# Kernel optimization log

Hardware: AMD Instinct MI355X
Metric: run time of the kernel (lower is better)

The kernel has to match this reference:

```python
import jax, jax.numpy as jnp
import numpy as np

N = 50000      # nodes
E = 800000     # edges
IN = 128       # in_channels
HID = 32       # hidden_channels per head
HEADS = 4
OUT = 16       # out_channels
NEG_SLOPE_ATT = 0.2   # GATv2Conv default negative_slope
NEG_SLOPE_ACT = 0.01  # F.leaky_relu default
EPS = 1e-16


def setup_inputs() -> dict:
    key = jax.random.key(0)
    ks = jax.random.split(key, 13)
    d1 = HEADS * HID  # 128
    g = lambda k, shape, fan: jax.random.normal(k, shape, jnp.float32) * (1.0 / np.sqrt(fan))
    return {
        "x": jax.random.normal(ks[0], (N, IN), jnp.float32),
        "edge_index": jax.random.randint(ks[1], (2, E), 0, N, dtype=jnp.int32),
        "edge_weight": jax.random.uniform(ks[2], (E,), jnp.float32),
        # conv1 (GATv2): lin_l, lin_r, att, bias
        "Wl1": g(ks[3], (IN, d1), IN), "Wr1": g(ks[4], (IN, d1), IN),
        "att1": g(ks[5], (HEADS, HID), HID), "b1": jnp.zeros((d1,), jnp.float32),
        # conv2
        "Wl2": g(ks[6], (d1, d1), d1), "Wr2": g(ks[7], (d1, d1), d1),
        "att2": g(ks[8], (HEADS, HID), HID), "b2": jnp.zeros((d1,), jnp.float32),
        # classifier
        "Wc": g(ks[9], (d1, OUT), d1), "bc": jnp.zeros((OUT,), jnp.float32),
    }


def gatv2_layer(x, Wl, Wr, att, bias, src, dst):
    n = x.shape[0]
    xl = (x @ Wl).reshape(n, HEADS, HID)  # source transform
    xr = (x @ Wr).reshape(n, HEADS, HID)  # target transform
    m = xl[src] + xr[dst]                                    # [Etot, H, C]
    e = jnp.sum(jax.nn.leaky_relu(m, NEG_SLOPE_ATT) * att, axis=-1)  # [Etot, H]
    # segment softmax over incoming edges of each target node
    emax = jax.ops.segment_max(e, dst, num_segments=n)       # [N, H]
    ex = jnp.exp(e - emax[dst])
    denom = jax.ops.segment_sum(ex, dst, num_segments=n)     # [N, H]
    alpha = ex / (denom[dst] + EPS)                          # [Etot, H]
    out = jax.ops.segment_sum(xl[src] * alpha[:, :, None], dst, num_segments=n)  # [N, H, C]
    return out.reshape(n, HEADS * HID) + bias


def reference(x, edge_index, edge_weight, Wl1, Wr1, att1, b1, Wl2, Wr2, att2, b2, Wc, bc):
    # GATv2Conv default add_self_loops=True
    loops = jnp.arange(N, dtype=edge_index.dtype)
    src = jnp.concatenate([edge_index[0], loops])
    dst = jnp.concatenate([edge_index[1], loops])
    h = gatv2_layer(x, Wl1, Wr1, att1, b1, src, dst)
    h = jax.nn.leaky_relu(h, NEG_SLOPE_ACT)
    h = gatv2_layer(h, Wl2, Wr2, att2, b2, src, dst)
    h = jax.nn.leaky_relu(h, NEG_SLOPE_ACT)
    logits = h @ Wc + bc
    return (logits, h)
```

## Files before the change

kernel.cpp:

```cpp
#include <hip/hip_runtime.h>
#include <hip/hip_fp16.h>


#define LOG2E 1.4426950408889634f
#define AST 40

typedef short bf16x8 __attribute__((ext_vector_type(8)));
typedef float f32x4 __attribute__((ext_vector_type(4)));

__device__ __forceinline__ unsigned short f2bf(float f) {
  union { float f; unsigned u; } x; x.f = f;
  unsigned r = x.u + 0x7fffu + ((x.u >> 16) & 1u);
  return (unsigned short)(r >> 16);
}
__device__ __forceinline__ float bf2f(unsigned short h) {
  union { unsigned u; float f; } x; x.u = ((unsigned)h) << 16;
  return x.f;
}
__device__ __forceinline__ void split4(float4 v, ushort4& h, ushort4& l) {
  h.x = f2bf(v.x); l.x = f2bf(v.x - bf2f(h.x));
  h.y = f2bf(v.y); l.y = f2bf(v.y - bf2f(h.y));
  h.z = f2bf(v.z); l.z = f2bf(v.z - bf2f(h.z));
  h.w = f2bf(v.w); l.w = f2bf(v.w - bf2f(h.w));
}


__global__ __launch_bounds__(256) void scan_blk(const int* __restrict__ cnt,
                                                int* __restrict__ excl,
                                                int* __restrict__ bsum, int n) {
  __shared__ int s[256];
  int t = threadIdx.x, i = blockIdx.x * 256 + t;
  int v = (i < n) ? (cnt[i] + 1) : 0;
  s[t] = v;
  __syncthreads();
#pragma unroll
  for (int off = 1; off < 256; off <<= 1) {
    int u = (t >= off) ? s[t - off] : 0;
    __syncthreads();
    s[t] += u;
    __syncthreads();
  }
  if (i < n) excl[i] = s[t] - v;
  if (t == 255) bsum[blockIdx.x] = s[255];
}

__global__ __launch_bounds__(256) void scan_bsum(int* __restrict__ bsum, int nb,
                                                 int* __restrict__ row_start, int n) {
  __shared__ int s[256];
  int t = threadIdx.x;
  int v = (t < nb) ? bsum[t] : 0;
  s[t] = v;
  __syncthreads();
#pragma unroll
  for (int off = 1; off < 256; off <<= 1) {
    int u = (t >= off) ? s[t - off] : 0;
    __syncthreads();
    s[t] += u;
    __syncthreads();
  }
  if (t < nb) bsum[t] = s[t] - v;
  if (t == 255) row_start[n] = s[255];
}

__global__ __launch_bounds__(256) void scan_add(int* __restrict__ row_start,
                                                const int* __restrict__ bsum,
                                                int* __restrict__ wpos,
                                                int* __restrict__ csr,
                                                int n, int padBase) {
  int i = blockIdx.x * 256 + threadIdx.x;
  if (i < n) {
    int r = row_start[i] + bsum[blockIdx.x];
    row_start[i] = r;
    wpos[i] = r + 1;
    csr[r] = i;
  }
  if (blockIdx.x == 0 && threadIdx.x < 16) csr[padBase + threadIdx.x] = 0;
}

#define EPB 1024
__global__ __launch_bounds__(256) void convert_count(
    const float* __restrict__ Wl1, const float* __restrict__ Wr1,
    const float* __restrict__ Wl2, const float* __restrict__ Wr2,
    unsigned short* __restrict__ BT1h, unsigned short* __restrict__ BT1l,
    unsigned short* __restrict__ BT2h, unsigned short* __restrict__ BT2l,
    const int* __restrict__ esrc, const int* __restrict__ edst,
    int* __restrict__ cnt, int* __restrict__ bucketCur,
    int2* __restrict__ bucket, int E, int sliceSize, int cap) {
  int b = blockIdx.x;
  int t = threadIdx.x;
  if (b >= 256) {
    __shared__ int bcnt[8], bbase[8];
    if (t < 8) bcnt[t] = 0;
    __syncthreads();
    int base = (b - 256) * EPB;
    int sl[4], rk[4], dv[4], sv[4];
#pragma unroll
    for (int j = 0; j < 4; ++j) {
      int i = base + t + j * 256;
      bool v = (i < E);
      int d = v ? edst[i] : 0;
      sv[j] = v ? esrc[i] : 0;
      dv[j] = d;
      int s = d / sliceSize;
      sl[j] = v ? s : -1;
      if (v) {
        atomicAdd(&cnt[d], 1);
        rk[j] = atomicAdd(&bcnt[s], 1);
      }
    }
    __syncthreads();
    if (t < 8 && bcnt[t] > 0) bbase[t] = atomicAdd(&bucketCur[t], bcnt[t]);
    __syncthreads();
#pragma unroll
    for (int j = 0; j < 4; ++j) {
      if (sl[j] >= 0) {
        int pos = sl[j] * cap + bbase[sl[j]] + rk[j];
        bucket[pos] = make_int2(sv[j], dv[j]);
      }
    }
    return;
  }
  const float* Wl = (b < 128) ? Wl1 : Wl2;
  const float* Wr = (b < 128) ? Wr1 : Wr2;
  unsigned short* BTh = (b < 128) ? BT1h : BT2h;
  unsigned short* BTl = (b < 128) ? BT1l : BT2l;
  int idx = (b & 127) * 256 + t;
  int col = idx >> 7, k = idx & 127;
  float v = (col < 128) ? Wl[k * 128 + col] : Wr[k * 128 + (col - 128)];
  unsigned short h = f2bf(v);
  BTh[idx] = h;
  BTl[idx] = f2bf(v - bf2f(h));
}

enum { IN_F32 = 0, IN_F16 = 1 };
#define NSCAT 1152
#define NCHUNK 128
template <int MODE, int FUSE>
__global__ __launch_bounds__(256) void gemm_mfma(
    const float* __restrict__ Af, const __half* __restrict__ Af16,
    const unsigned short* __restrict__ BTh, const unsigned short* __restrict__ BTl,
    __half* __restrict__ Cl, __half* __restrict__ Cr, int nrows,
    const int2* __restrict__ bucket, const int* __restrict__ bucketCur,
    int* __restrict__ wpos, int* __restrict__ csr, int cap) {
  __shared__ __align__(16) unsigned short smem[4 * 128 * AST];
  int tid = threadIdx.x;
  int bx, by;
  if (FUSE) {
    int g = blockIdx.x / 9, r = blockIdx.x - g * 9;
    if (r < 5) {
      int sid = g * 5 + r;
      if (sid < NSCAT) {
        int slice = blockIdx.x & 7;
        int chunk = (g >> 3) * 5;
        for (int gp = g & ~7; gp < g; ++gp)
          chunk += (((slice - gp) & 7) < 5) ? 1 : 0;
        if (chunk < NCHUNK) {
          int cntS = bucketCur[slice];
          int per = (cntS + NCHUNK - 1) / NCHUNK;
          int b0 = chunk * per;
          int ee = min(b0 + per, cntS);
          const int2* bk = bucket + (size_t)slice * cap;
          int i = b0 + tid;
          for (; i + 256 < ee; i += 512) {
            int2 e0 = bk[i];
            int2 e1 = bk[i + 256];
            int p0 = atomicAdd(&wpos[e0.y], 1); csr[p0] = e0.x;
            int p1 = atomicAdd(&wpos[e1.y], 1); csr[p1] = e1.x;
          }
          for (; i < ee; i += 256) {
            int2 e = bk[i];
            int p = atomicAdd(&wpos[e.y], 1); csr[p] = e.x;
          }
        }
      }
      return;
    }
    int gid = g * 4 + (r - 5);
    int nbx = (nrows + 127) >> 7;
    if (gid >= nbx * 2) return;
    bx = gid >> 1;
    by = gid & 1;
  } else {
    bx = blockIdx.x;
    by = blockIdx.y;
  }

  unsigned short* sAh = smem;
  unsigned short* sAl = smem + 5120;
  unsigned short* sBh = smem + 10240;
  unsigned short* sBl = smem + 15360;

  int wave = tid >> 6, lane = tid & 63;
  int rowBase = bx * 128;
  int colBase = by * 128;
  int rowHalf = (wave >> 1) * 64;
  int colHalf = (wave & 1) * 64;
  int l15 = lane & 15, quad = lane >> 4;

  f32x4 acc[4][4];
#pragma unroll
  for (int m = 0; m < 4; ++m)
#pragma unroll
    for (int n = 0; n < 4; ++n) acc[m][n] = (f32x4){0.f, 0.f, 0.f, 0.f};

  for (int kc = 0; kc < 4; ++kc) {
#pragma unroll
    for (int i = 0; i < 2; ++i) {
      int idx = tid + i * 256;
      int row = idx >> 2, seg = idx & 3;
      int gr = rowBase + row;
      float4 v0 = make_float4(0.f, 0.f, 0.f, 0.f), v1 = v0;
      if (MODE == IN_F32) {
        if (gr < nrows) {
          v0 = *(const float4*)&Af[(size_t)gr * 128 + kc * 32 + seg * 8];
          v1 = *(const float4*)&Af[(size_t)gr * 128 + kc * 32 + seg * 8 + 4];
        }
      } else {
        if (gr < nrows) {
          uint4 raw = *(const uint4*)&Af16[(size_t)gr * 128 + kc * 32 + seg * 8];
          const __half* hp = (const __half*)&raw;
          v0 = make_float4(__half2float(hp[0]), __half2float(hp[1]),
                           __half2float(hp[2]), __half2float(hp[3]));
          v1 = make_float4(__half2float(hp[4]), __half2float(hp[5]),
                           __half2float(hp[6]), __half2float(hp[7]));
        }
      }
      ushort4 h0, l0, h1, l1;
      split4(v0, h0, l0);
      split4(v1, h1, l1);
      *(ushort4*)&sAh[row * AST + seg * 8] = h0;
      *(ushort4*)&sAh[row * AST + seg * 8 + 4] = h1;
      *(ushort4*)&sAl[row * AST + seg * 8] = l0;
      *(ushort4*)&sAl[row * AST + seg * 8 + 4] = l1;
    }
#pragma unroll
    for (int i = 0; i < 2; ++i) {
      int idx = tid + i * 256;
      int col = idx >> 2, seg = idx & 3;
      *(uint4*)&sBh[col * AST + seg * 8] =
          *(const uint4*)&BTh[(size_t)(colBase + col) * 128 + kc * 32 + seg * 8];
      *(uint4*)&sBl[col * AST + seg * 8] =
          *(const uint4*)&BTl[(size_t)(colBase + col) * 128 + kc * 32 + seg * 8];
    }
    __syncthreads();

    bf16x8 afh[4], afl[4], bfh[4], bfl[4];
#pragma unroll
    for (int m = 0; m < 4; ++m) {
      int r = rowHalf + m * 16 + l15;
      afh[m] = *(const bf16x8*)&sAh[r * AST + quad * 8];
      afl[m] = *(const bf16x8*)&sAl[r * AST + quad * 8];
    }
#pragma unroll
    for (int n = 0; n < 4; ++n) {
      int cc = colHalf + n * 16 + l15;
      bfh[n] = *(const bf16x8*)&sBh[cc * AST + quad * 8];
      bfl[n] = *(const bf16x8*)&sBl[cc * AST + quad * 8];
    }
    __builtin_amdgcn_s_setprio(1);
#pragma unroll
    for (int m = 0; m < 4; ++m)
#pragma unroll
      for (int n = 0; n < 4; ++n) {
        acc[m][n] = __builtin_amdgcn_mfma_f32_16x16x32_bf16(afh[m], bfh[n], acc[m][n], 0, 0, 0);
        acc[m][n] = __builtin_amdgcn_mfma_f32_16x16x32_bf16(afh[m], bfl[n], acc[m][n], 0, 0, 0);
        acc[m][n] = __builtin_amdgcn_mfma_f32_16x16x32_bf16(afl[m], bfh[n], acc[m][n], 0, 0, 0);
      }
    __builtin_amdgcn_s_setprio(0);
    __syncthreads();
  }

  __half* __restrict__ C = (by == 0) ? Cl : Cr;
#pragma unroll
  for (int m = 0; m < 4; ++m)
#pragma unroll
    for (int r = 0; r < 4; ++r) {
      int grow = rowBase + rowHalf + m * 16 + quad * 4 + r;
      if (grow < nrows) {
#pragma unroll
        for (int n = 0; n < 4; ++n)
          C[(size_t)grow * 128 + colHalf + n * 16 + l15] = __float2half(acc[m][n][r]);
      }
    }
}

__global__ __launch_bounds__(256) void gat_attn(const __half* __restrict__ xl,
                                                const __half* __restrict__ xr,
                                                const int* __restrict__ row_start,
                                                const int* __restrict__ csr,
                                                const float* __restrict__ att,
                                                const float* __restrict__ bias,
                                                float* __restrict__ ofp,
                                                __half* __restrict__ oh16,
                                                int n_nodes) {
  int node = blockIdx.x * 4 + (threadIdx.x >> 6);
  if (node >= n_nodes) return;
  int lane = threadIdx.x & 63;
  int slot = lane >> 4;
  int l15 = lane & 15;
  int c0 = l15 * 8;

  float fxr[8];
  {
    uint4 raw = *(const uint4*)&xr[(size_t)node * 128 + c0];
    const __half* hp = (const __half*)&raw;
#pragma unroll
    for (int k = 0; k < 8; ++k) fxr[k] = __half2float(hp[k]);
  }
  float a06[8], a04[8];
  {
    float4 a0 = *(const float4*)&att[c0];
    float4 a1 = *(const float4*)&att[c0 + 4];
    float av[8] = {a0.x, a0.y, a0.z, a0.w, a1.x, a1.y, a1.z, a1.w};
    const float C06 = 0.6f * LOG2E, C04 = 0.4f * LOG2E;
#pragma unroll
    for (int k = 0; k < 8; ++k) { a06[k] = av[k] * C06; a04[k] = av[k] * C04; }
  }

  float acc[8];
#pragma unroll
  for (int k = 0; k < 8; ++k) acc[k] = 0.f;
  float lsum = 0.f;

#define EDGE_BODY(SRC, PVALID)                                                 \
  {                                                                            \
    uint4 raw = *(const uint4*)&xl[(size_t)(unsigned)(SRC)*128 + c0];          \
    const __half* hp = (const __half*)&raw;                                    \
    float e = 0.f;                                                             \
    _Pragma("unroll") for (int k = 0; k < 8; ++k) {                            \
      float t = __half2float(hp[k]) + fxr[k];                                  \
      e = fmaf(a06[k], t, e);                                                  \
      e = fmaf(a04[k], fabsf(t), e);                                           \
    }                                                                          \
    e += __shfl_xor(e, 1);                                                     \
    e += __shfl_xor(e, 2);                                                     \
    float p = (PVALID) ? __builtin_amdgcn_exp2f(e) : 0.f;                      \
    lsum += p;                                                                 \
    _Pragma("unroll") for (int k = 0; k < 8; ++k)                              \
        acc[k] = fmaf(p, __half2float(hp[k]), acc[k]);                         \
  }

  int beg = row_start[node], end = row_start[node + 1];
  int deg = end - beg;
  int fullEnd = beg + (deg & ~15);

  for (int base = beg; base < fullEnd; base += 16) {
    int b0 = base + 4 * slot;
    int s0 = csr[b0], s1 = csr[b0 + 1], s2 = csr[b0 + 2], s3 = csr[b0 + 3];
    EDGE_BODY(s0, true);
    EDGE_BODY(s1, true);
    EDGE_BODY(s2, true);
    EDGE_BODY(s3, true);
  }
  for (int base = fullEnd; base < end; base += 4) {
    int idx = base + slot;
    int src = csr[idx];
    EDGE_BODY(src, idx < end);
  }
#undef EDGE_BODY

  lsum += __shfl_xor(lsum, 16);
  lsum += __shfl_xor(lsum, 32);
#pragma unroll
  for (int k = 0; k < 8; ++k) {
    acc[k] += __shfl_xor(acc[k], 16);
    acc[k] += __shfl_xor(acc[k], 32);
  }

  if (slot == 0) {
    float4 b0v = *(const float4*)&bias[c0];
    float4 b1v = *(const float4*)&bias[c0 + 4];
    float bv[8] = {b0v.x, b0v.y, b0v.z, b0v.w, b1v.x, b1v.y, b1v.z, b1v.w};
    float inv = 1.f / (lsum + 1e-16f);
    float o[8];
#pragma unroll
    for (int k = 0; k < 8; ++k) {
      float v = fmaf(acc[k], inv, bv[k]);
      o[k] = fmaf(0.495f, fabsf(v), 0.505f * v);
    }
    if (ofp) {
      *(float4*)&ofp[(size_t)node * 128 + c0] = make_float4(o[0], o[1], o[2], o[3]);
      *(float4*)&ofp[(size_t)node * 128 + c0 + 4] = make_float4(o[4], o[5], o[6], o[7]);
    }
    if (oh16) {
      ushort4 ha, hb;
      ha.x = __half_as_ushort(__float2half(o[0]));
      ha.y = __half_as_ushort(__float2half(o[1]));
      ha.z = __half_as_ushort(__float2half(o[2]));
      ha.w = __half_as_ushort(__float2half(o[3]));
      hb.x = __half_as_ushort(__float2half(o[4]));
      hb.y = __half_as_ushort(__float2half(o[5]));
      hb.z = __half_as_ushort(__float2half(o[6]));
      hb.w = __half_as_ushort(__float2half(o[7]));
      *(ushort4*)&oh16[(size_t)node * 128 + c0] = ha;
      *(ushort4*)&oh16[(size_t)node * 128 + c0 + 4] = hb;
    }
  }
}

__global__ __launch_bounds__(256) void classifier_kernel(const float4* __restrict__ h4,
                                                         const float* __restrict__ Wc,
                                                         const float* __restrict__ bc,
                                                         float* __restrict__ logits,
                                                         int n) {
  __shared__ float sW[2048];
  __shared__ float sb[16];
  int t = threadIdx.x;
#pragma unroll
  for (int i = 0; i < 8; ++i) sW[t + i * 256] = Wc[t + i * 256];
  if (t < 16) sb[t] = bc[t];
  __syncthreads();
  int node = blockIdx.x * 256 + t;
  if (node >= n) return;
  float acc[16];
#pragma unroll
  for (int o = 0; o < 16; ++o) acc[o] = sb[o];
  for (int c4 = 0; c4 < 32; ++c4) {
    float4 hv = h4[(unsigned)node * 32 + c4];
    const float* w = &sW[c4 * 64];
#pragma unroll
    for (int o = 0; o < 16; ++o) {
      acc[o] = fmaf(hv.x, w[o], acc[o]);
      acc[o] = fmaf(hv.y, w[16 + o], acc[o]);
      acc[o] = fmaf(hv.z, w[32 + o], acc[o]);
      acc[o] = fmaf(hv.w, w[48 + o], acc[o]);
    }
  }
#pragma unroll
  for (int q = 0; q < 4; ++q)
    *(float4*)&logits[(size_t)node * 16 + q * 4] =
        make_float4(acc[q * 4], acc[q * 4 + 1], acc[q * 4 + 2], acc[q * 4 + 3]);
}


extern "C" void kernel_launch(void* const* d_in, const int* in_sizes, int n_in,
                              void* d_out, int out_size, void* d_ws, size_t ws_size,
                              hipStream_t stream) {
  const float* x    = (const float*)d_in[0];
  const int*   ei   = (const int*)d_in[1];
  const float* Wl1  = (const float*)d_in[3];
  const float* Wr1  = (const float*)d_in[4];
  const float* att1 = (const float*)d_in[5];
  const float* b1   = (const float*)d_in[6];
  const float* Wl2  = (const float*)d_in[7];
  const float* Wr2  = (const float*)d_in[8];
  const float* att2 = (const float*)d_in[9];
  const float* b2   = (const float*)d_in[10];
  const float* Wc   = (const float*)d_in[11];
  const float* bc   = (const float*)d_in[12];

  const int N = in_sizes[0] / 128;
  const int E = in_sizes[1] / 2;

  float* outp   = (float*)d_out;
  float* logits = outp;
  float* hout   = outp + (size_t)N * 16;
  __half* h1f16 = (__half*)hout;

  const int cap = E / 8 + 16384;

  char* ws = (char*)d_ws;
  __half* xlbuf = (__half*)ws;                ws += (size_t)N * 128 * 2;
  __half* xrbuf = (__half*)ws;                ws += (size_t)N * 128 * 2;
  unsigned short* WT1h = (unsigned short*)ws; ws += 256 * 128 * 2;
  unsigned short* WT1l = (unsigned short*)ws; ws += 256 * 128 * 2;
  unsigned short* WT2h = (unsigned short*)ws; ws += 256 * 128 * 2;
  unsigned short* WT2l = (unsigned short*)ws; ws += 256 * 128 * 2;
  int* cnt       = (int*)ws;                  ws += (size_t)N * 4;
  int* bucketCur = (int*)ws;                  ws += 8 * 4;
  int* wpos      = (int*)ws;                  ws += (size_t)N * 4;
  int* bsum      = (int*)ws;                  ws += 256 * 4;
  int2* bucket   = (int2*)ws;                 ws += (size_t)8 * cap * 8;
  int* row_start = (int*)ws;                  ws += (size_t)(N + 1) * 4;
  int* csr       = (int*)ws;                  ws += (size_t)(E + N + 16) * 4;

  const int* esrc = ei;
  const int* edst = ei + E;

  int gN = (N + 255) / 256;
  int gAttn = (N + 3) / 4;
  int sliceSize = (N + 7) / 8;

  int nbx = (N + 127) / 128;
  int nGemm = nbx * 2;
  int groups = (NSCAT + 4) / 5;
  int g2 = (nGemm + 3) / 4;
  if (g2 > groups) groups = g2;
  int gFused = groups * 9;

  hipMemsetAsync(cnt, 0, (size_t)(N + 8) * 4, stream);
  convert_count<<<256 + (E + EPB - 1) / EPB, 256, 0, stream>>>(
      Wl1, Wr1, Wl2, Wr2, WT1h, WT1l, WT2h, WT2l,
      esrc, edst, cnt, bucketCur, bucket, E, sliceSize, cap);
  scan_blk<<<gN, 256, 0, stream>>>(cnt, row_start, bsum, N);
  scan_bsum<<<1, 256, 0, stream>>>(bsum, gN, row_start, N);
  scan_add<<<gN, 256, 0, stream>>>(row_start, bsum, wpos, csr, N, E + N);

  gemm_mfma<IN_F32, 1><<<gFused, 256, 0, stream>>>(
      x, nullptr, WT1h, WT1l, xlbuf, xrbuf, N,
      bucket, bucketCur, wpos, csr, cap);
  gat_attn<<<gAttn, 256, 0, stream>>>(xlbuf, xrbuf, row_start, csr, att1, b1,
                                      nullptr, h1f16, N);

  gemm_mfma<IN_F16, 0><<<dim3(nbx, 2), 256, 0, stream>>>(
      nullptr, h1f16, WT2h, WT2l, xlbuf, xrbuf, N,
      nullptr, nullptr, nullptr, nullptr, 0);
  gat_attn<<<gAttn, 256, 0, stream>>>(xlbuf, xrbuf, row_start, csr, att2, b2,
                                      hout, nullptr, N);

  classifier_kernel<<<(N + 255) / 256, 256, 0, stream>>>((const float4*)hout, Wc, bc,
                                                         logits, N);
}
```

Baseline: 307.0 us.

## Interleave CSR edge scatter into GEMM blocks and merge the scan kernels

Previously the first GEMM launch had dedicated scatter blocks in a 5:4 interleave. Now every GEMM block preloads its share of the bucketed edges into registers before its k-loop. It issues the wpos atomics after the first k-iteration and the csr stores after the second, so the atomic latency hides behind MFMA work. Separately, the single-block scan_bsum kernel is removed: each scan_add block redundantly scans the block sums in shared memory, saving one launch. The per-block edge capacity is fixed at 5×256, so a slice with more edges than the grid can hold would silently drop edges. The extra registers held across the k-loop may also affect occupancy.

```diff
diff --git a/kernel.cpp b/kernel.cpp
--- a/kernel.cpp
+++ b/kernel.cpp
@@ -44,8 +44,11 @@
   if (t == 255) bsum[blockIdx.x] = s[255];
 }
 
-__global__ __launch_bounds__(256) void scan_bsum(int* __restrict__ bsum, int nb,
-                                                 int* __restrict__ row_start, int n) {
+__global__ __launch_bounds__(256) void scan_add(int* __restrict__ row_start,
+                                                const int* __restrict__ bsum,
+                                                int* __restrict__ wpos,
+                                                int* __restrict__ csr,
+                                                int n, int padBase, int nb) {
   __shared__ int s[256];
   int t = threadIdx.x;
   int v = (t < nb) ? bsum[t] : 0;
@@ -58,23 +61,18 @@
     s[t] += u;
     __syncthreads();
   }
-  if (t < nb) bsum[t] = s[t] - v;
-  if (t == 255) row_start[n] = s[255];
-}
-
-__global__ __launch_bounds__(256) void scan_add(int* __restrict__ row_start,
-                                                const int* __restrict__ bsum,
-                                                int* __restrict__ wpos,
-                                                int* __restrict__ csr,
-                                                int n, int padBase) {
-  int i = blockIdx.x * 256 + threadIdx.x;
+  int pref = (blockIdx.x > 0) ? s[blockIdx.x - 1] : 0;
+  int i = blockIdx.x * 256 + t;
   if (i < n) {
-    int r = row_start[i] + bsum[blockIdx.x];
+    int r = row_start[i] + pref;
     row_start[i] = r;
     wpos[i] = r + 1;
     csr[r] = i;
   }
-  if (blockIdx.x == 0 && threadIdx.x < 16) csr[padBase + threadIdx.x] = 0;
+  if (blockIdx.x == 0) {
+    if (t == 0) row_start[n] = s[nb - 1];
+    if (t < 16) csr[padBase + t] = 0;
+  }
 }
 
 #define EPB 1024
@@ -133,8 +131,7 @@
 }
 
 enum { IN_F32 = 0, IN_F16 = 1 };
-#define NSCAT 1152
-#define NCHUNK 128
+#define SJ 5
 template <int MODE, int FUSE>
 __global__ __launch_bounds__(256) void gemm_mfma(
     const float* __restrict__ Af, const __half* __restrict__ Af16,
@@ -145,39 +142,33 @@
   __shared__ __align__(16) unsigned short smem[4 * 128 * AST];
   int tid = threadIdx.x;
   int bx, by;
+  int2 ebuf[SJ];
+  int epos[SJ];
   if (FUSE) {
-    int g = blockIdx.x / 9, r = blockIdx.x - g * 9;
-    if (r < 5) {
-      int sid = g * 5 + r;
-      if (sid < NSCAT) {
-        int slice = blockIdx.x & 7;
-        int chunk = (g >> 3) * 5;
-        for (int gp = g & ~7; gp < g; ++gp)
-          chunk += (((slice - gp) & 7) < 5) ? 1 : 0;
-        if (chunk < NCHUNK) {
-          int cntS = bucketCur[slice];
-          int per = (cntS + NCHUNK - 1) / NCHUNK;
-          int b0 = chunk * per;
-          int ee = min(b0 + per, cntS);
-          const int2* bk = bucket + (size_t)slice * cap;
-          int i = b0 + tid;
-          for (; i + 256 < ee; i += 512) {
-            int2 e0 = bk[i];
-            int2 e1 = bk[i + 256];
-            int p0 = atomicAdd(&wpos[e0.y], 1); csr[p0] = e0.x;
-            int p1 = atomicAdd(&wpos[e1.y], 1); csr[p1] = e1.x;
-          }
-          for (; i < ee; i += 256) {
-            int2 e = bk[i];
-            int p = atomicAdd(&wpos[e.y], 1); csr[p] = e.x;
-          }
+    int gid = blockIdx.x;
+    int slice = gid & 7;
+    int rank = gid >> 3;
+    int nbs = (int)(gridDim.x >> 3);
+    int cntS = bucketCur[slice];
+    int per = (cntS + nbs - 1) / nbs;
+    int b0 = rank * per;
+    int ee = min(b0 + per, cntS);
+    const int2* bk = bucket + (size_t)slice * cap;
+#pragma unroll
+    for (int j = 0; j < SJ; ++j) {
+      int idx = b0 + tid + j * 256;
+      ebuf[j] = (idx < ee) ? bk[idx] : make_int2(0, -1);
+    }
+    int nbx = (nrows + 127) >> 7;
+    if (gid >= nbx * 2) {
+#pragma unroll
+      for (int j = 0; j < SJ; ++j)
+        if (ebuf[j].y >= 0) {
+          int p = atomicAdd(&wpos[ebuf[j].y], 1);
+          csr[p] = ebuf[j].x;
         }
-      }
       return;
     }
-    int gid = g * 4 + (r - 5);
-    int nbx = (nrows + 127) >> 7;
-    if (gid >= nbx * 2) return;
     bx = gid >> 1;
     by = gid & 1;
   } else {
@@ -268,6 +259,18 @@
       }
     __builtin_amdgcn_s_setprio(0);
     __syncthreads();
+
+    if (FUSE) {
+      if (kc == 0) {
+#pragma unroll
+        for (int j = 0; j < SJ; ++j)
+          epos[j] = (ebuf[j].y >= 0) ? atomicAdd(&wpos[ebuf[j].y], 1) : -1;
+      } else if (kc == 1) {
+#pragma unroll
+        for (int j = 0; j < SJ; ++j)
+          if (epos[j] >= 0) csr[epos[j]] = ebuf[j].x;
+      }
+    }
   }
 
   __half* __restrict__ C = (by == 0) ? Cl : Cr;
@@ -483,18 +486,14 @@
 
   int nbx = (N + 127) / 128;
   int nGemm = nbx * 2;
-  int groups = (NSCAT + 4) / 5;
-  int g2 = (nGemm + 3) / 4;
-  if (g2 > groups) groups = g2;
-  int gFused = groups * 9;
+  int gFused = (nGemm + 7) & ~7;
 
   hipMemsetAsync(cnt, 0, (size_t)(N + 8) * 4, stream);
   convert_count<<<256 + (E + EPB - 1) / EPB, 256, 0, stream>>>(
       Wl1, Wr1, Wl2, Wr2, WT1h, WT1l, WT2h, WT2l,
       esrc, edst, cnt, bucketCur, bucket, E, sliceSize, cap);
   scan_blk<<<gN, 256, 0, stream>>>(cnt, row_start, bsum, N);
-  scan_bsum<<<1, 256, 0, stream>>>(bsum, gN, row_start, N);
-  scan_add<<<gN, 256, 0, stream>>>(row_start, bsum, wpos, csr, N, E + N);
+  scan_add<<<gN, 256, 0, stream>>>(row_start, bsum, wpos, csr, N, E + N, gN);
 
   gemm_mfma<IN_F32, 1><<<gFused, 256, 0, stream>>>(
       x, nullptr, WT1h, WT1l, xlbuf, xrbuf, N,
```

Result: slower. 318.9 us (+3.9%).

## Switch split GEMM to fp16 MFMA, skip A-low term for fp16 input, merge scans

Applied to the files above, without the earlier changes.

Replaces the bf16 hi/lo split with an fp16 hi/lo split and uses fp16 MFMA. For the second-layer GEMM, whose input is already fp16, the A operand is copied directly to shared memory without conversion, dropping the A-low buffer and one of three MFMAs per tile. Separately, the block-sum scan is folded into scan_add: every block redundantly scans the block sums itself, saving one kernel launch. The risk is fp16 range and precision: weights and x whose magnitude exceeds fp16 range, or small residuals that underflow, could lose accuracy.

```diff
diff --git a/kernel.cpp b/kernel.cpp
--- a/kernel.cpp
+++ b/kernel.cpp
@@ -5,7 +5,7 @@
 #define LOG2E 1.4426950408889634f
 #define AST 40
 
-typedef short bf16x8 __attribute__((ext_vector_type(8)));
+typedef _Float16 f16x8 __attribute__((ext_vector_type(8)));
 typedef float f32x4 __attribute__((ext_vector_type(4)));
 
 __device__ __forceinline__ unsigned short f2bf(float f) {
@@ -17,11 +17,13 @@
   union { unsigned u; float f; } x; x.u = ((unsigned)h) << 16;
   return x.f;
 }
-__device__ __forceinline__ void split4(float4 v, ushort4& h, ushort4& l) {
-  h.x = f2bf(v.x); l.x = f2bf(v.x - bf2f(h.x));
-  h.y = f2bf(v.y); l.y = f2bf(v.y - bf2f(h.y));
-  h.z = f2bf(v.z); l.z = f2bf(v.z - bf2f(h.z));
-  h.w = f2bf(v.w); l.w = f2bf(v.w - bf2f(h.w));
+__device__ __forceinline__ void split4h(float4 v, ushort4& h, ushort4& l) {
+  __half hx = __float2half(v.x), hy = __float2half(v.y);
+  __half hz = __float2half(v.z), hw = __float2half(v.w);
+  h.x = __half_as_ushort(hx); l.x = __half_as_ushort(__float2half(v.x - __half2float(hx)));
+  h.y = __half_as_ushort(hy); l.y = __half_as_ushort(__float2half(v.y - __half2float(hy)));
+  h.z = __half_as_ushort(hz); l.z = __half_as_ushort(__float2half(v.z - __half2float(hz)));
+  h.w = __half_as_ushort(hw); l.w = __half_as_ushort(__float2half(v.w - __half2float(hw)));
 }
 
 
@@ -44,8 +46,11 @@
   if (t == 255) bsum[blockIdx.x] = s[255];
 }
 
-__global__ __launch_bounds__(256) void scan_bsum(int* __restrict__ bsum, int nb,
-                                                 int* __restrict__ row_start, int n) {
+__global__ __launch_bounds__(256) void scan_add(int* __restrict__ row_start,
+                                                const int* __restrict__ bsum,
+                                                int* __restrict__ wpos,
+                                                int* __restrict__ csr,
+                                                int n, int padBase, int nb) {
   __shared__ int s[256];
   int t = threadIdx.x;
   int v = (t < nb) ? bsum[t] : 0;
@@ -58,23 +63,18 @@
     s[t] += u;
     __syncthreads();
   }
-  if (t < nb) bsum[t] = s[t] - v;
-  if (t == 255) row_start[n] = s[255];
-}
-
-__global__ __launch_bounds__(256) void scan_add(int* __restrict__ row_start,
-                                                const int* __restrict__ bsum,
-                                                int* __restrict__ wpos,
-                                                int* __restrict__ csr,
-                                                int n, int padBase) {
-  int i = blockIdx.x * 256 + threadIdx.x;
+  int pref = (blockIdx.x > 0) ? s[blockIdx.x - 1] : 0;
+  int i = blockIdx.x * 256 + t;
   if (i < n) {
-    int r = row_start[i] + bsum[blockIdx.x];
+    int r = row_start[i] + pref;
     row_start[i] = r;
     wpos[i] = r + 1;
     csr[r] = i;
   }
-  if (blockIdx.x == 0 && threadIdx.x < 16) csr[padBase + threadIdx.x] = 0;
+  if (blockIdx.x == 0) {
+    if (t == 0) row_start[n] = s[nb - 1];
+    if (t < 16) csr[padBase + t] = 0;
+  }
 }
 
 #define EPB 1024
@@ -127,9 +127,9 @@
   int idx = (b & 127) * 256 + t;
   int col = idx >> 7, k = idx & 127;
   float v = (col < 128) ? Wl[k * 128 + col] : Wr[k * 128 + (col - 128)];
-  unsigned short h = f2bf(v);
-  BTh[idx] = h;
-  BTl[idx] = f2bf(v - bf2f(h));
+  __half h = __float2half(v);
+  BTh[idx] = __half_as_ushort(h);
+  BTl[idx] = __half_as_ushort(__float2half(v - __half2float(h)));
 }
 
 enum { IN_F32 = 0, IN_F16 = 1 };
@@ -142,7 +142,8 @@
     __half* __restrict__ Cl, __half* __restrict__ Cr, int nrows,
     const int2* __restrict__ bucket, const int* __restrict__ bucketCur,
     int* __restrict__ wpos, int* __restrict__ csr, int cap) {
-  __shared__ __align__(16) unsigned short smem[4 * 128 * AST];
+  constexpr int NBUF = (MODE == IN_F16) ? 3 : 4;
+  __shared__ __align__(16) unsigned short smem[NBUF * 128 * AST];
   int tid = threadIdx.x;
   int bx, by;
   if (FUSE) {
@@ -185,10 +186,11 @@
     by = blockIdx.y;
   }
 
+  constexpr int ABUF = 128 * AST;
   unsigned short* sAh = smem;
-  unsigned short* sAl = smem + 5120;
-  unsigned short* sBh = smem + 10240;
-  unsigned short* sBl = smem + 15360;
+  unsigned short* sAl = (MODE == IN_F32) ? smem + ABUF : nullptr;
+  unsigned short* sBh = smem + ((MODE == IN_F32) ? 2 * ABUF : ABUF);
+  unsigned short* sBl = smem + ((MODE == IN_F32) ? 3 * ABUF : 2 * ABUF);
 
   int wave = tid >> 6, lane = tid & 63;
   int rowBase = bx * 128;
@@ -209,29 +211,25 @@
       int idx = tid + i * 256;
       int row = idx >> 2, seg = idx & 3;
       int gr = rowBase + row;
-      float4 v0 = make_float4(0.f, 0.f, 0.f, 0.f), v1 = v0;
       if (MODE == IN_F32) {
+        float4 v0 = make_float4(0.f, 0.f, 0.f, 0.f), v1 = v0;
         if (gr < nrows) {
           v0 = *(const float4*)&Af[(size_t)gr * 128 + kc * 32 + seg * 8];
           v1 = *(const float4*)&Af[(size_t)gr * 128 + kc * 32 + seg * 8 + 4];
         }
+        ushort4 h0, l0, h1, l1;
+        split4h(v0, h0, l0);
+        split4h(v1, h1, l1);
+        *(ushort4*)&sAh[row * AST + seg * 8] = h0;
+        *(ushort4*)&sAh[row * AST + seg * 8 + 4] = h1;
+        *(ushort4*)&sAl[row * AST + seg * 8] = l0;
+        *(ushort4*)&sAl[row * AST + seg * 8 + 4] = l1;
       } else {
-        if (gr < nrows) {
-          uint4 raw = *(const uint4*)&Af16[(size_t)gr * 128 + kc * 32 + seg * 8];
-          const __half* hp = (const __half*)&raw;
-          v0 = make_float4(__half2float(hp[0]), __half2float(hp[1]),
-                           __half2float(hp[2]), __half2float(hp[3]));
-          v1 = make_float4(__half2float(hp[4]), __half2float(hp[5]),
-                           __half2float(hp[6]), __half2float(hp[7]));
-        }
+        uint4 raw = make_uint4(0, 0, 0, 0);
+        if (gr < nrows)
+          raw = *(const uint4*)&Af16[(size_t)gr * 128 + kc * 32 + seg * 8];
+        *(uint4*)&sAh[row * AST + seg * 8] = raw;
       }
-      ushort4 h0, l0, h1, l1;
-      split4(v0, h0, l0);
-      split4(v1, h1, l1);
-      *(ushort4*)&sAh[row * AST + seg * 8] = h0;
-      *(ushort4*)&sAh[row * AST + seg * 8 + 4] = h1;
-      *(ushort4*)&sAl[row * AST + seg * 8] = l0;
-      *(ushort4*)&sAl[row * AST + seg * 8 + 4] = l1;
     }
 #pragma unroll
     for (int i = 0; i < 2; ++i) {
@@ -244,27 +242,28 @@
     }
     __syncthreads();
 
-    bf16x8 afh[4], afl[4], bfh[4], bfl[4];
+    f16x8 afh[4], afl[4], bfh[4], bfl[4];
 #pragma unroll
     for (int m = 0; m < 4; ++m) {
       int r = rowHalf + m * 16 + l15;
-      afh[m] = *(const bf16x8*)&sAh[r * AST + quad * 8];
-      afl[m] = *(const bf16x8*)&sAl[r * AST + quad * 8];
+      afh[m] = *(const f16x8*)&sAh[r * AST + quad * 8];
+      if (MODE == IN_F32) afl[m] = *(const f16x8*)&sAl[r * AST + quad * 8];
     }
 #pragma unroll
     for (int n = 0; n < 4; ++n) {
       int cc = colHalf + n * 16 + l15;
-      bfh[n] = *(const bf16x8*)&sBh[cc * AST + quad * 8];
-      bfl[n] = *(const bf16x8*)&sBl[cc * AST + quad * 8];
+      bfh[n] = *(const f16x8*)&sBh[cc * AST + quad * 8];
+      bfl[n] = *(const f16x8*)&sBl[cc * AST + quad * 8];
     }
     __builtin_amdgcn_s_setprio(1);
 #pragma unroll
     for (int m = 0; m < 4; ++m)
 #pragma unroll
       for (int n = 0; n < 4; ++n) {
-        acc[m][n] = __builtin_amdgcn_mfma_f32_16x16x32_bf16(afh[m], bfh[n], acc[m][n], 0, 0, 0);
-        acc[m][n] = __builtin_amdgcn_mfma_f32_16x16x32_bf16(afh[m], bfl[n], acc[m][n], 0, 0, 0);
-        acc[m][n] = __builtin_amdgcn_mfma_f32_16x16x32_bf16(afl[m], bfh[n], acc[m][n], 0, 0, 0);
+        acc[m][n] = __builtin_amdgcn_mfma_f32_16x16x32_f16(afh[m], bfh[n], acc[m][n], 0, 0, 0);
+        acc[m][n] = __builtin_amdgcn_mfma_f32_16x16x32_f16(afh[m], bfl[n], acc[m][n], 0, 0, 0);
+        if (MODE == IN_F32)
+          acc[m][n] = __builtin_amdgcn_mfma_f32_16x16x32_f16(afl[m], bfh[n], acc[m][n], 0, 0, 0);
       }
     __builtin_amdgcn_s_setprio(0);
     __syncthreads();
@@ -493,8 +492,7 @@
       Wl1, Wr1, Wl2, Wr2, WT1h, WT1l, WT2h, WT2l,
       esrc, edst, cnt, bucketCur, bucket, E, sliceSize, cap);
   scan_blk<<<gN, 256, 0, stream>>>(cnt, row_start, bsum, N);
-  scan_bsum<<<1, 256, 0, stream>>>(bsum, gN, row_start, N);
-  scan_add<<<gN, 256, 0, stream>>>(row_start, bsum, wpos, csr, N, E + N);
+  scan_add<<<gN, 256, 0, stream>>>(row_start, bsum, wpos, csr, N, E + N, gN);
 
   gemm_mfma<IN_F32, 1><<<gFused, 256, 0, stream>>>(
       x, nullptr, WT1h, WT1l, xlbuf, xrbuf, N,
```

Result: no change. 303.6 us (-1.1%).
